# Performance work log

Measured on AMD Instinct MI355X. Metric: run time of the kernel, lower is better.

Reference implementation:

```python
import jax, jax.numpy as jnp
import numpy as np

B, L, E, H, W = 2, 8192, 1024, 16, 128
HD = E // H  # 64


def setup_inputs() -> dict:
    key = jax.random.key(0)
    ks = jax.random.split(key, 9)
    s = 1.0 / np.sqrt(E)
    inp = {"x": jax.random.normal(ks[0], (B, L, E), jnp.float32)}
    for i, n in enumerate(["Wq", "Wk", "Wv", "Wo"]):
        inp[n] = jax.random.uniform(ks[1 + i], (E, E), jnp.float32, -s, s)
    for i, n in enumerate(["bq", "bk", "bv", "bo"]):
        inp[n] = jax.random.uniform(ks[5 + i], (E,), jnp.float32, -s, s)
    return inp


def _skew_prob(p, w):
    # (..., w, 2w+1) -> (..., w, 3w) with row i right-shifted by i:
    # out[..., i, i+j] = p[..., i, j]  (zeros elsewhere)
    lead = p.shape[:-2]
    M, Lc = p.shape[-2], p.shape[-1]
    p = jnp.pad(p, [(0, 0)] * len(lead) + [(0, 0), (0, M + 1)])
    p = p.reshape(*lead, M * (Lc + M + 1))[..., :-M].reshape(*lead, M, M + Lc)
    return p[..., :-1]


def _sliding_attend(q, k, v, w):
    # q,k,v: (b,h,l,d); banded attention, window w on each side (2w+1 diagonals)
    b, h, l, d = q.shape
    c = l // w
    qc = q.reshape(b, h, c, w, d)
    # per-chunk key/value windows of 3w tokens (w halo each side, zero padded)
    idx = jnp.arange(c)[:, None] * w + jnp.arange(3 * w)[None, :]  # (c, 3w)
    kw = jnp.pad(k, ((0, 0), (0, 0), (w, w), (0, 0)))[:, :, idx]  # (b,h,c,3w,d)
    s = jnp.einsum('bhcqd,bhckd->bhcqk', qc, kw)  # (b,h,c,w,3w)
    # extract band: band[i, j] = s[i, i+j], j in [0, 2w] (offset d = j - w)
    gidx = (jnp.arange(w)[:, None] + jnp.arange(2 * w + 1)[None, :])[None, None, None]
    band = jnp.take_along_axis(s, gidx, axis=-1).reshape(b, h, l, 2 * w + 1)
    # mask out-of-range positions (matches the module's edge -inf loop)
    pos = jnp.arange(l)[:, None] + (jnp.arange(2 * w + 1) - w)[None, :]
    band = jnp.where((pos >= 0) & (pos < l), band, -jnp.inf)
    prob = jax.nn.softmax(band / np.sqrt(d), axis=-1)  # scale by sqrt(head_dim)
    vw = jnp.pad(v, ((0, 0), (0, 0), (w, w), (0, 0)))[:, :, idx]  # (b,h,c,3w,d)
    p3 = _skew_prob(prob.reshape(b, h, c, w, 2 * w + 1), w)  # (b,h,c,w,3w)
    ctx = jnp.einsum('bhcqk,bhckd->bhcqd', p3, vw)
    return ctx.reshape(b, h, l, d)


def reference(x, Wq, Wk, Wv, Wo, bq, bk, bv, bo):
    q = (x @ Wq.T + bq).reshape(B, L, H, HD).transpose(0, 2, 1, 3)
    k = (x @ Wk.T + bk).reshape(B, L, H, HD).transpose(0, 2, 1, 3)
    v = (x @ Wv.T + bv).reshape(B, L, H, HD).transpose(0, 2, 1, 3)
    ctx = _sliding_attend(q, k, v, W)
    ctx = ctx.transpose(0, 2, 1, 3).reshape(B, L, E)
    return ctx @ Wo.T + bo
```

## Files before the change

kernel.cpp:

```cpp
#include <hip/hip_runtime.h>
#include <math.h>

#define B_SZ  2
#define L_SEQ 8192
#define EMB   1024
#define NH    16
#define HDIM  64
#define WIN   128
#define MROWS (B_SZ*L_SEQ)

typedef __attribute__((ext_vector_type(8))) _Float16 f16x8;
typedef __attribute__((ext_vector_type(4))) _Float16 f16x4;
typedef __attribute__((ext_vector_type(4))) float f32x4;

__device__ __forceinline__ void gload16(const void* g, void* l) {
    __builtin_amdgcn_global_load_lds(
        (const __attribute__((address_space(1))) unsigned int*)g,
        (__attribute__((address_space(3))) unsigned int*)l, 16, 0, 0);
}

__global__ __launch_bounds__(256)
void round_all(const float* __restrict__ x,
               const float* __restrict__ wq, const float* __restrict__ wk,
               const float* __restrict__ wv, const float* __restrict__ wo,
               _Float16* __restrict__ xf, _Float16* __restrict__ q16,
               _Float16* __restrict__ k16, _Float16* __restrict__ v16,
               _Float16* __restrict__ o16)
{
    const size_t NX = (size_t)MROWS * EMB, NW = (size_t)EMB * EMB;
    size_t gid = ((size_t)blockIdx.x * 256 + threadIdx.x) * 4;
    const float* src; _Float16* dst; size_t off;
    if (gid < NX)               { src = x;  dst = xf;  off = gid; }
    else if (gid < NX + NW)     { src = wq; dst = q16; off = gid - NX; }
    else if (gid < NX + 2*NW)   { src = wk; dst = k16; off = gid - NX - 2*NW + NW; }
    else if (gid < NX + 3*NW)   { src = wv; dst = v16; off = gid - NX - 2*NW; }
    else                        { src = wo; dst = o16; off = gid - NX - 3*NW; }
    float4 v = *(const float4*)(src + off);
    f16x4 o;
    o[0] = (_Float16)v.x; o[1] = (_Float16)v.y;
    o[2] = (_Float16)v.z; o[3] = (_Float16)v.w;
    *(f16x4*)(dst + off) = o;
}


#define STAGE_HT(ptr_, tb_, op_, h_, kt_)                                      \
    {                                                                          \
        char* d_ = smem + (op_) * 65536 + ((kt_) & 1) * 32768 + (h_) * 16384 + ldst; \
        const _Float16* s_ = (ptr_) + ((size_t)((tb_) + (h_) * 128 + srow6)) * 1024 + (kt_) * 64 + gch; \
        gload16(s_, d_);                                                       \
        gload16(s_ + 64 * 1024, d_ + 8192);                                    \
    }

#define DSREAD_A(qr_)                                                          \
    _Pragma("unroll")                                                          \
    for (int i_ = 0; i_ < 4; ++i_) {                                           \
        const int ro_ = (qr_) * 8192 + (i_ * 16 + frow) * 128;                 \
        af[i_][0] = *(const f16x8*)(Ab + ro_ + sb0);                           \
        af[i_][1] = *(const f16x8*)(Ab + ro_ + sb1);                           \
    }

#define DSREAD_B_TO(dst_, qc_)                                                 \
    _Pragma("unroll")                                                          \
    for (int j_ = 0; j_ < 2; ++j_) {                                           \
        const int ro_ = (brow + (qc_) * 32 + j_ * 16 + frow) * 128;            \
        dst_[j_][0] = *(const f16x8*)(Bb + ro_ + sb0);                         \
        dst_[j_][1] = *(const f16x8*)(Bb + ro_ + sb1);                         \
    }

#define MFMA16(qr_, qc_, barr_)                                                \
    __builtin_amdgcn_s_setprio(1);                                             \
    _Pragma("unroll")                                                          \
    for (int ks_ = 0; ks_ < 2; ++ks_)                                          \
        _Pragma("unroll")                                                      \
        for (int i_ = 0; i_ < 4; ++i_)                                         \
            _Pragma("unroll")                                                  \
            for (int j_ = 0; j_ < 2; ++j_)                                     \
                acc[(qr_) * 4 + i_][(qc_) * 2 + j_] =                          \
                    __builtin_amdgcn_mfma_f32_16x16x32_f16(                    \
                        af[i_][ks_], barr_[j_][ks_],                           \
                        acc[(qr_) * 4 + i_][(qc_) * 2 + j_], 0, 0, 0);         \
    __builtin_amdgcn_s_setprio(0);

#define BARM()                                                                 \
    asm volatile("" ::: "memory");                                             \
    __builtin_amdgcn_s_barrier();                                              \
    asm volatile("" ::: "memory");

#define GEMM8_CORE(Aptr, Bptr)                                                 \
    const int t = threadIdx.x;                                                 \
    const int wave = t >> 6, lane = t & 63;                                    \
    const int wr = wave >> 2, wc = wave & 3;                                   \
    const int frow = lane & 15, quad = lane >> 4;                              \
    const int srow6 = t >> 3;                                                  \
    const int gch = ((t & 7) ^ (srow6 & 7)) * 8;                               \
    const int ldst = t * 16;                                                   \
    const int sb0 = (quad ^ (frow & 7)) * 16, sb1 = sb0 ^ 64;                  \
    const int brow = (wc & 1) * 64;                                            \
    f32x4 acc[8][4] = {};                                                      \
    f16x8 af[4][2], bfA[2][2], bfB[2][2];                                      \
    STAGE_HT(Aptr, bm, 0, 0, 0) STAGE_HT(Aptr, bm, 0, 1, 0)                    \
    STAGE_HT(Bptr, bn, 1, 0, 0) STAGE_HT(Bptr, bn, 1, 1, 0)                    \
    for (int kt = 0; kt < 16; ++kt) {                                          \
        const char* Ab = smem + (kt & 1) * 32768 + wr * 16384;                 \
        const char* Bb = smem + 65536 + (kt & 1) * 32768 + (wc >> 1) * 16384;  \
        if (kt < 15) {                                                         \
            STAGE_HT(Aptr, bm, 0, 0, kt + 1)                                   \
            asm volatile("s_waitcnt vmcnt(2)" ::: "memory");                   \
        } else {                                                               \
            asm volatile("s_waitcnt vmcnt(0)" ::: "memory");                   \
        }                                                                      \
        BARM()                                                                 \
        DSREAD_A(0) DSREAD_B_TO(bfA, 0)          \
        MFMA16(0, 0, bfA)                                                      \
        DSREAD_B_TO(bfB, 1)                    \
        if (kt < 15) STAGE_HT(Aptr, bm, 0, 1, kt + 1)                          \
        BARM()                                                                 \
        MFMA16(0, 1, bfB)                                                      \
        DSREAD_A(1)                                                            \
        if (kt < 15) STAGE_HT(Bptr, bn, 1, 0, kt + 1)                          \
        BARM()                                                                 \
        MFMA16(1, 1, bfB)                                                      \
        if (kt < 15) STAGE_HT(Bptr, bn, 1, 1, kt + 1)                          \
        BARM()                                                                 \
        MFMA16(1, 0, bfA)                     \
        BARM()                                                                 \
    }

__global__ __launch_bounds__(512, 2)
void gemm_qkv(const _Float16* __restrict__ X,
              const _Float16* __restrict__ Wq, const _Float16* __restrict__ Wk,
              const _Float16* __restrict__ Wv,
              const float* __restrict__ bq, const float* __restrict__ bk,
              const float* __restrict__ bv,
              _Float16* __restrict__ qf, _Float16* __restrict__ kf,
              _Float16* __restrict__ vtf)
{
    __shared__ __attribute__((aligned(16))) char smem[131072];

    const int id = blockIdx.x;
    const int row = (id / 96) * 8 + (id & 7);
    const int colq = (id >> 3) % 12;
    const int wsel = colq >> 2;
    const int bm = row * 256, bn = (colq & 3) * 256;
    const _Float16* Bw = wsel == 0 ? Wq : wsel == 1 ? Wk : Wv;
    const float* bias = wsel == 0 ? bq : wsel == 1 ? bk : bv;
    const float scale = wsel == 0 ? 0.125f : 1.0f;

    GEMM8_CORE(X, Bw)

    char* Cw = smem + wave * 8192;
    const int bb = bm >> 13;
    const int l0 = (bm & (L_SEQ - 1)) + wr * 128;
    const int h = (bn >> 6) + wc;
    if (wsel < 2) {
        _Float16* dst = wsel == 0 ? qf : kf;
        const size_t hb = ((size_t)(bb * NH + h)) * L_SEQ * HDIM;
        #pragma unroll
        for (int ih = 0; ih < 2; ++ih) {
            asm volatile("" ::: "memory");
            #pragma unroll
            for (int i = 0; i < 4; ++i)
                #pragma unroll
                for (int j = 0; j < 4; ++j) {
                    const int lc = j * 16 + frow;
                    const float bvv = bias[bn + wc * 64 + lc];
                    #pragma unroll
                    for (int r = 0; r < 4; ++r) {
                        const int lr = i * 16 + quad * 4 + r;
                        const int bo = lr * 128 + ((lc * 2) ^ ((lr & 7) << 4));
                        *(_Float16*)(Cw + bo) = (_Float16)((acc[ih * 4 + i][j][r] + bvv) * scale);
                    }
                }
            asm volatile("" ::: "memory");
            #pragma unroll
            for (int p = 0; p < 8; ++p) {
                const int idx = p * 64 + lane;
                const int lr = idx >> 3, seg = idx & 7;
                const int bo = lr * 128 + ((seg * 16) ^ ((lr & 7) << 4));
                uint4 v = *(const uint4*)(Cw + bo);
                *(uint4*)&dst[hb + (size_t)(l0 + ih * 64 + lr) * HDIM + seg * 8] = v;
            }
        }
    } else {
        const size_t hb = ((size_t)(bb * NH + h)) * HDIM * L_SEQ;
        #pragma unroll
        for (int ih = 0; ih < 2; ++ih) {
            asm volatile("" ::: "memory");
            #pragma unroll
            for (int i = 0; i < 4; ++i)
                #pragma unroll
                for (int j = 0; j < 4; ++j) {
                    const int lc = j * 16 + frow;
                    const float bvv = bias[bn + wc * 64 + lc];
                    #pragma unroll
                    for (int r = 0; r < 4; ++r) {
                        const int lr = i * 16 + quad * 4 + r;
                        const int bo = lc * 128 + ((lr * 2) ^ ((lc & 7) << 4));
                        *(_Float16*)(Cw + bo) = (_Float16)(acc[ih * 4 + i][j][r] + bvv);
                    }
                }
            asm volatile("" ::: "memory");
            #pragma unroll
            for (int p = 0; p < 8; ++p) {
                const int idx = p * 64 + lane;
                const int dc = idx >> 3, sl = idx & 7;
                const int bo = dc * 128 + ((sl * 16) ^ ((dc & 7) << 4));
                uint4 v = *(const uint4*)(Cw + bo);
                *(uint4*)&vtf[hb + (size_t)dc * L_SEQ + (l0 + ih * 64 + sl * 8)] = v;
            }
        }
    }
}

__global__ __launch_bounds__(512, 2)
void gemm_out(const _Float16* __restrict__ A, const _Float16* __restrict__ Bwm,
              const float* __restrict__ bias, float* __restrict__ C)
{
    constexpr int N = EMB;
    __shared__ __attribute__((aligned(16))) char smem[131072];

    const int id = blockIdx.x;
    const int row = (id / 32) * 8 + (id & 7);
    const int bm = row * 256, bn = ((id >> 3) & 3) * 256;

    GEMM8_CORE(A, Bwm)

    #pragma unroll
    for (int i = 0; i < 8; ++i) {
        int m0 = bm + wr * 128 + i * 16 + quad * 4;
        #pragma unroll
        for (int j = 0; j < 4; ++j) {
            int n = bn + wc * 64 + j * 16 + frow;
            float bvv = bias[n];
            #pragma unroll
            for (int r = 0; r < 4; ++r)
                C[(size_t)(m0 + r) * N + n] = acc[i][j][r] + bvv;
        }
    }
}

__global__ __launch_bounds__(512)
void attn_mfma(const _Float16* __restrict__ qf, const _Float16* __restrict__ kf,
               const _Float16* __restrict__ vtf, _Float16* __restrict__ cf)
{
    __shared__ _Float16 Kf[2][4096], Vf[2][4096];

    const int t = threadIdx.x;
    const int wave = t >> 6, lane = t & 63;
    const int col = lane & 15, quad = lane >> 4;
    const int bh = blockIdx.y;
    const int q0 = blockIdx.x * 128;
    const int oo = wave * 16;

    f16x8 qfr[2];
    {
        size_t qidx = ((size_t)bh * L_SEQ + q0 + oo + col) * HDIM + quad * 8;
        qfr[0] = *(const f16x8*)(qf + qidx);
        qfr[1] = *(const f16x8*)(qf + qidx + 32);
    }

    f32x4 o[4] = {};
    float lsum = 0.0f;

    const int srow = t >> 3, sc = t & 7;

    const int ktlo = (q0 == 0) ? 2 : 0;
    const int kthi = (q0 == L_SEQ - 128) ? 4 : 6;

#define STAGE_KV(kt_, bsel_)                                                   \
    {                                                                          \
        const int p0s = q0 - WIN + (kt_) * 64;                                 \
        const int gq = sc ^ (srow & 7);                                        \
        size_t kgi = ((size_t)bh * L_SEQ + p0s + srow) * HDIM + gq * 8;        \
        size_t vgi = ((size_t)bh * HDIM + srow) * L_SEQ + p0s + gq * 8;        \
        gload16(kf + kgi, (char*)&Kf[bsel_][0] + t * 16);                      \
        gload16(vtf + vgi, (char*)&Vf[bsel_][0] + t * 16);                     \
    }

    STAGE_KV(ktlo, 0)

    for (int kt = ktlo; kt < kthi; kt++) {
        const int p0 = q0 - WIN + kt * 64;
        const int cb = (kt - ktlo) & 1;
        if (kt + 1 < kthi) {
            STAGE_KV(kt + 1, cb ^ 1)
            asm volatile("s_waitcnt vmcnt(2)" ::: "memory");
        } else {
            asm volatile("s_waitcnt vmcnt(0)" ::: "memory");
        }
        __builtin_amdgcn_s_barrier();
        asm volatile("" ::: "memory");

        const char* Kb = (const char*)&Kf[cb][0];
        const char* Vb = (const char*)&Vf[cb][0];

        const int relp = kt * 64 - WIN - oo;
        if (relp >= -191 && relp <= 143) {
            f32x4 sT[4] = {};
            #pragma unroll
            for (int ks = 0; ks < 2; ks++)
                #pragma unroll
                for (int n = 0; n < 4; n++) {
                    int off = (n * 16 + col) * 128 + (((ks * 4 + quad) ^ (col & 7)) * 16);
                    f16x8 kfr = *(const f16x8*)(Kb + off);
                    sT[n] = __builtin_amdgcn_mfma_f32_16x16x32_f16(kfr, qfr[ks], sT[n], 0, 0, 0);
                }
            if (relp < -113 || relp > 65) {
                const int qrow = q0 + oo + col;
                #pragma unroll
                for (int n = 0; n < 4; n++)
                    #pragma unroll
                    for (int r = 0; r < 4; r++) {
                        int dlt = (p0 + n * 16 + quad * 4 + r) - qrow;
                        if (dlt < -WIN || dlt > WIN) sT[n][r] = -3e38f;
                    }
            }
            f16x4 pT[4];
            #pragma unroll
            for (int n = 0; n < 4; n++)
                #pragma unroll
                for (int r = 0; r < 4; r++) {
                    float pv = __expf(sT[n][r]);
                    lsum += pv;
                    pT[n][r] = (_Float16)pv;
                }
            #pragma unroll
            for (int m = 0; m < 4; m++) {
                #pragma unroll
                for (int n = 0; n < 4; n++) {
                    int off = (m * 16 + col) * 128 +
                              (((2 * n + (quad >> 1)) ^ (col & 7)) * 16) + (quad & 1) * 8;
                    f16x4 vfr = *(const f16x4*)(Vb + off);
                    o[m] = __builtin_amdgcn_mfma_f32_16x16x16f16(vfr, pT[n], o[m], 0, 0, 0);
                }
            }
        }
        asm volatile("" ::: "memory");
        __builtin_amdgcn_s_barrier();
        asm volatile("" ::: "memory");
    }

    lsum += __shfl_xor(lsum, 16, 64);
    lsum += __shfl_xor(lsum, 32, 64);
    const float inv = 1.0f / lsum;

    const int b = bh >> 4, h = bh & 15;
    const size_t base = ((size_t)b * L_SEQ + q0 + oo + col) * EMB + h * HDIM;
    #pragma unroll
    for (int m = 0; m < 4; m++) {
        f16x4 ov;
        #pragma unroll
        for (int r = 0; r < 4; r++) ov[r] = (_Float16)(o[m][r] * inv);
        *(f16x4*)&cf[base + m * 16 + quad * 4] = ov;
    }
}

extern "C" void kernel_launch(void* const* d_in, const int* in_sizes, int n_in,
                              void* d_out, int out_size, void* d_ws, size_t ws_size,
                              hipStream_t stream) {
    const float* x  = (const float*)d_in[0];
    const float* Wq = (const float*)d_in[1];
    const float* Wk = (const float*)d_in[2];
    const float* Wv = (const float*)d_in[3];
    const float* Wo = (const float*)d_in[4];
    const float* bq = (const float*)d_in[5];
    const float* bk = (const float*)d_in[6];
    const float* bv = (const float*)d_in[7];
    const float* bo = (const float*)d_in[8];
    float* out = (float*)d_out;

    const size_t per = (size_t)B_SZ * NH * L_SEQ * HDIM;
    _Float16* w16 = (_Float16*)d_ws;
    _Float16* xf   = w16;
    _Float16* qf   = w16 + per;
    _Float16* kf   = w16 + 2 * per;
    _Float16* vtf  = w16 + 3 * per;
    _Float16* cf   = w16 + 4 * per;
    _Float16* wq16 = w16 + 5 * per;
    _Float16* wk16 = wq16 + 1048576;
    _Float16* wv16 = wq16 + 2 * 1048576;
    _Float16* wo16 = wq16 + 3 * 1048576;

    const int nround = (MROWS * EMB + 4 * EMB * EMB) / 1024;
    round_all<<<nround, dim3(256), 0, stream>>>(x, Wq, Wk, Wv, Wo, xf, wq16, wk16, wv16, wo16);

    gemm_qkv<<<768, dim3(512), 0, stream>>>(xf, wq16, wk16, wv16, bq, bk, bv, qf, kf, vtf);

    attn_mfma<<<dim3(L_SEQ / 128, B_SZ * NH), dim3(512), 0, stream>>>(qf, kf, vtf, cf);

    gemm_out<<<256, dim3(512), 0, stream>>>(cf, wo16, bo, out);
}
```

Measured before the change: 318.5 us.

## Split QKV GEMM into three launches and preload whole K/V window in attention

The fused QKV projection is split into three separate 256-block launches, one per weight matrix, each selected by a kernel argument. The attention kernel now loads all six K/V tiles into shared memory up front with a single wait and barrier, replacing the double-buffered loop that synchronised on every tile. It also swizzles the query-block order so neighbouring blocks are spread across the sequence. This trades per-tile barriers for a larger shared-memory footprint (96 KB), which may lower occupancy, and adds launch overhead from two extra kernels.

```diff
diff --git a/kernel.cpp b/kernel.cpp
--- a/kernel.cpp
+++ b/kernel.cpp
@@ -133,15 +133,13 @@
               const float* __restrict__ bq, const float* __restrict__ bk,
               const float* __restrict__ bv,
               _Float16* __restrict__ qf, _Float16* __restrict__ kf,
-              _Float16* __restrict__ vtf)
+              _Float16* __restrict__ vtf, const int wsel)
 {
     __shared__ __attribute__((aligned(16))) char smem[131072];
 
     const int id = blockIdx.x;
-    const int row = (id / 96) * 8 + (id & 7);
-    const int colq = (id >> 3) % 12;
-    const int wsel = colq >> 2;
-    const int bm = row * 256, bn = (colq & 3) * 256;
+    const int row = (id / 32) * 8 + (id & 7);
+    const int bm = row * 256, bn = ((id >> 3) & 3) * 256;
     const _Float16* Bw = wsel == 0 ? Wq : wsel == 1 ? Wk : Wv;
     const float* bias = wsel == 0 ? bq : wsel == 1 ? bk : bv;
     const float scale = wsel == 0 ? 0.125f : 1.0f;
@@ -243,14 +241,29 @@
 void attn_mfma(const _Float16* __restrict__ qf, const _Float16* __restrict__ kf,
                const _Float16* __restrict__ vtf, _Float16* __restrict__ cf)
 {
-    __shared__ _Float16 Kf[2][4096], Vf[2][4096];
+    __shared__ _Float16 Kt[6][4096];
+    __shared__ _Float16 Vt[6][4096];
 
     const int t = threadIdx.x;
     const int wave = t >> 6, lane = t & 63;
     const int col = lane & 15, quad = lane >> 4;
     const int bh = blockIdx.y;
-    const int q0 = blockIdx.x * 128;
+    const int xi = blockIdx.x;
+    const int xq = (xi & 7) * 8 + (xi >> 3);
+    const int q0 = xq * 128;
     const int oo = wave * 16;
+
+    const int srow = t >> 3, sc = t & 7;
+    const int gq = sc ^ (srow & 7);
+    #pragma unroll
+    for (int kt = 0; kt < 6; kt++) {
+        const int p0s = q0 - WIN + kt * 64;
+        if (p0s < 0 || p0s >= L_SEQ) continue;
+        size_t kgi = ((size_t)bh * L_SEQ + p0s + srow) * HDIM + gq * 8;
+        size_t vgi = ((size_t)bh * HDIM + srow) * L_SEQ + p0s + gq * 8;
+        gload16(kf + kgi, (char*)&Kt[kt][0] + t * 16);
+        gload16(vtf + vgi, (char*)&Vt[kt][0] + t * 16);
+    }
 
     f16x8 qfr[2];
     {
@@ -259,85 +272,61 @@
         qfr[1] = *(const f16x8*)(qf + qidx + 32);
     }
 
+    asm volatile("s_waitcnt vmcnt(0)" ::: "memory");
+    __builtin_amdgcn_s_barrier();
+    asm volatile("" ::: "memory");
+
     f32x4 o[4] = {};
     float lsum = 0.0f;
 
-    const int srow = t >> 3, sc = t & 7;
-
-    const int ktlo = (q0 == 0) ? 2 : 0;
-    const int kthi = (q0 == L_SEQ - 128) ? 4 : 6;
-
-#define STAGE_KV(kt_, bsel_)                                                   \
-    {                                                                          \
-        const int p0s = q0 - WIN + (kt_) * 64;                                 \
-        const int gq = sc ^ (srow & 7);                                        \
-        size_t kgi = ((size_t)bh * L_SEQ + p0s + srow) * HDIM + gq * 8;        \
-        size_t vgi = ((size_t)bh * HDIM + srow) * L_SEQ + p0s + gq * 8;        \
-        gload16(kf + kgi, (char*)&Kf[bsel_][0] + t * 16);                      \
-        gload16(vtf + vgi, (char*)&Vf[bsel_][0] + t * 16);                     \
-    }
-
-    STAGE_KV(ktlo, 0)
-
-    for (int kt = ktlo; kt < kthi; kt++) {
+    #pragma unroll
+    for (int kt = 0; kt < 6; kt++) {
         const int p0 = q0 - WIN + kt * 64;
-        const int cb = (kt - ktlo) & 1;
-        if (kt + 1 < kthi) {
-            STAGE_KV(kt + 1, cb ^ 1)
-            asm volatile("s_waitcnt vmcnt(2)" ::: "memory");
-        } else {
-            asm volatile("s_waitcnt vmcnt(0)" ::: "memory");
-        }
-        __builtin_amdgcn_s_barrier();
-        asm volatile("" ::: "memory");
-
-        const char* Kb = (const char*)&Kf[cb][0];
-        const char* Vb = (const char*)&Vf[cb][0];
-
+        if (p0 < 0 || p0 >= L_SEQ) continue;
         const int relp = kt * 64 - WIN - oo;
-        if (relp >= -191 && relp <= 143) {
-            f32x4 sT[4] = {};
-            #pragma unroll
-            for (int ks = 0; ks < 2; ks++)
-                #pragma unroll
-                for (int n = 0; n < 4; n++) {
-                    int off = (n * 16 + col) * 128 + (((ks * 4 + quad) ^ (col & 7)) * 16);
-                    f16x8 kfr = *(const f16x8*)(Kb + off);
-                    sT[n] = __builtin_amdgcn_mfma_f32_16x16x32_f16(kfr, qfr[ks], sT[n], 0, 0, 0);
-                }
-            if (relp < -113 || relp > 65) {
-                const int qrow = q0 + oo + col;
-                #pragma unroll
-                for (int n = 0; n < 4; n++)
-                    #pragma unroll
-                    for (int r = 0; r < 4; r++) {
-                        int dlt = (p0 + n * 16 + quad * 4 + r) - qrow;
-                        if (dlt < -WIN || dlt > WIN) sT[n][r] = -3e38f;
-                    }
-            }
-            f16x4 pT[4];
+        if (relp < -191 || relp > 143) continue;
+
+        const char* Kb = (const char*)&Kt[kt][0];
+        const char* Vb = (const char*)&Vt[kt][0];
+
+        f32x4 sT[4] = {};
+        #pragma unroll
+        for (int ks = 0; ks < 2; ks++)
+            #pragma unroll
+            for (int n = 0; n < 4; n++) {
+                int off = (n * 16 + col) * 128 + (((ks * 4 + quad) ^ (col & 7)) * 16);
+                f16x8 kfr = *(const f16x8*)(Kb + off);
+                sT[n] = __builtin_amdgcn_mfma_f32_16x16x32_f16(kfr, qfr[ks], sT[n], 0, 0, 0);
+            }
+        if (relp < -113 || relp > 65) {
+            const int qrow = q0 + oo + col;
             #pragma unroll
             for (int n = 0; n < 4; n++)
                 #pragma unroll
                 for (int r = 0; r < 4; r++) {
-                    float pv = __expf(sT[n][r]);
-                    lsum += pv;
-                    pT[n][r] = (_Float16)pv;
+                    int dlt = (p0 + n * 16 + quad * 4 + r) - qrow;
+                    if (dlt < -WIN || dlt > WIN) sT[n][r] = -3e38f;
                 }
-            #pragma unroll
-            for (int m = 0; m < 4; m++) {
-                #pragma unroll
-                for (int n = 0; n < 4; n++) {
-                    int off = (m * 16 + col) * 128 +
-                              (((2 * n + (quad >> 1)) ^ (col & 7)) * 16) + (quad & 1) * 8;
-                    f16x4 vfr = *(const f16x4*)(Vb + off);
-                    o[m] = __builtin_amdgcn_mfma_f32_16x16x16f16(vfr, pT[n], o[m], 0, 0, 0);
-                }
-            }
-        }
-        asm volatile("" ::: "memory");
-        __builtin_amdgcn_s_barrier();
-        asm volatile("" ::: "memory");
+        }
+        f16x4 pT[4];
+        #pragma unroll
+        for (int n = 0; n < 4; n++)
+            #pragma unroll
+            for (int r = 0; r < 4; r++) {
+                float pv = __expf(sT[n][r]);
+                lsum += pv;
+                pT[n][r] = (_Float16)pv;
+            }
+        #pragma unroll
+        for (int m = 0; m < 4; m++) {
+            #pragma unroll
+            for (int n = 0; n < 4; n++) {
+                int off = (m * 16 + col) * 128 +
+                          (((2 * n + (quad >> 1)) ^ (col & 7)) * 16) + (quad & 1) * 8;
+                f16x4 vfr = *(const f16x4*)(Vb + off);
+                o[m] = __builtin_amdgcn_mfma_f32_16x16x16f16(vfr, pT[n], o[m], 0, 0, 0);
+            }
+        }
     }
 
     lsum += __shfl_xor(lsum, 16, 64);
@@ -384,7 +373,9 @@
     const int nround = (MROWS * EMB + 4 * EMB * EMB) / 1024;
     round_all<<<nround, dim3(256), 0, stream>>>(x, Wq, Wk, Wv, Wo, xf, wq16, wk16, wv16, wo16);
 
-    gemm_qkv<<<768, dim3(512), 0, stream>>>(xf, wq16, wk16, wv16, bq, bk, bv, qf, kf, vtf);
+    gemm_qkv<<<256, dim3(512), 0, stream>>>(xf, wq16, wk16, wv16, bq, bk, bv, qf, kf, vtf, 0);
+    gemm_qkv<<<256, dim3(512), 0, stream>>>(xf, wq16, wk16, wv16, bq, bk, bv, qf, kf, vtf, 1);
+    gemm_qkv<<<256, dim3(512), 0, stream>>>(xf, wq16, wk16, wv16, bq, bk, bv, qf, kf, vtf, 2);
 
     attn_mfma<<<dim3(L_SEQ / 128, B_SZ * NH), dim3(512), 0, stream>>>(qf, kf, vtf, cf);
 
```

After: 334.2 us. 1.05x slower.
